# Kernel optimization log

Measured on AMD Instinct MI355X. Metric: run time of the kernel, lower is better.

Reference implementation:

```python
import jax, jax.numpy as jnp
import numpy as np

B, S, D, H = 8, 1024, 256, 16
HD = D // H  # head_dim = 16
THETA = 10000.0


def rope(x):
    # Faithful to RotaryEmbeddings: integer-division exponent, 1-indexed
    # positions, rotor = sin + i*cos (real part is sin).
    b, s, d = x.shape
    i = jnp.arange(0, d, 2)
    expo = (2 * i) // d  # integer division: 0 for first half, 1 for second
    thetas = 1.0 / (THETA ** expo.astype(jnp.float32))  # [d/2]
    pos = jnp.arange(s, dtype=jnp.float32) + 1.0  # 1-indexed positions
    ang = pos[:, None] * thetas[None, :]  # [s, d/2]
    sin, cos = jnp.sin(ang), jnp.cos(ang)
    xp = x.reshape(b, s, d // 2, 2)
    xe, xo = xp[..., 0], xp[..., 1]  # consecutive pairs (view_as_complex)
    # (xe + i*xo) * (sin + i*cos)
    real = xe * sin - xo * cos
    imag = xe * cos + xo * sin
    return jnp.stack((real, imag), axis=-1).reshape(b, s, d)


def setup_inputs() -> dict:
    key = jax.random.key(0)
    ks = jax.random.split(key, 9)
    sc = 1.0 / np.sqrt(D)
    return {
        "x": jax.random.normal(ks[0], (B, S, D), dtype=jnp.float32),
        "wq_w": jax.random.normal(ks[1], (D, D), dtype=jnp.float32) * sc,
        "wq_b": jax.random.normal(ks[2], (D,), dtype=jnp.float32) * 0.01,
        "wk_w": jax.random.normal(ks[3], (D, D), dtype=jnp.float32) * sc,
        "wk_b": jax.random.normal(ks[4], (D,), dtype=jnp.float32) * 0.01,
        "wv_w": jax.random.normal(ks[5], (D, D), dtype=jnp.float32) * sc,
        "wv_b": jax.random.normal(ks[6], (D,), dtype=jnp.float32) * 0.01,
        "wo_w": jax.random.normal(ks[7], (D, D), dtype=jnp.float32) * sc,
        "wo_b": jax.random.normal(ks[8], (D,), dtype=jnp.float32) * 0.01,
    }


def reference(x, wq_w, wq_b, wk_w, wk_b, wv_w, wv_b, wo_w, wo_b):
    b, s, d = x.shape
    q = x @ wq_w.T + wq_b
    k = x @ wk_w.T + wk_b  # computed in original but dead in no-cache path
    v = x @ wv_w.T + wv_b
    del k
    xq = rope(q).reshape(b, s, H, HD).transpose(0, 2, 1, 3)  # [b,h,s,hd]
    xv = rope(v).reshape(b, s, H, HD).transpose(0, 2, 1, 3)  # [b,h,s,hd]
    # no-cache path: keys = xq (rotated queries), values = rotated v; NO softmax
    scores = jnp.einsum('bhqd,bhkd->bhqk', xq, xq) / jnp.sqrt(jnp.float32(HD))
    att = jnp.einsum('bhqk,bhkd->bhqd', scores, xv)  # [b,h,s,hd]
    att = att.transpose(0, 2, 1, 3).reshape(b, s, d)
    return att @ wo_w.T + wo_b
```

## Files before the change

### kernel.cpp

```cpp
#include <hip/hip_runtime.h>

#define Gz 8192
#define Dz 256
#define Sz 1024

typedef _Float16 half8 __attribute__((ext_vector_type(8)));
typedef float    floatx4 __attribute__((ext_vector_type(4)));

#define GLOAD_LDS(gptr, lptr)                                                      \
    __builtin_amdgcn_global_load_lds(                                              \
        (const __attribute__((address_space(1))) void*)(gptr),                     \
        (__attribute__((address_space(3))) void*)(lptr), 16, 0, 0)

__device__ inline half8 cvt8(const float* __restrict__ p) {
    float4 a = ((const float4*)p)[0];
    float4 b = ((const float4*)p)[1];
    half8 h;
    h[0]=(_Float16)a.x; h[1]=(_Float16)a.y; h[2]=(_Float16)a.z; h[3]=(_Float16)a.w;
    h[4]=(_Float16)b.x; h[5]=(_Float16)b.y; h[6]=(_Float16)b.z; h[7]=(_Float16)b.w;
    return h;
}

__global__ __launch_bounds__(256) void convert_kernel(
    const float* __restrict__ x, const float* __restrict__ wq,
    const float* __restrict__ wv,
    _Float16* __restrict__ x16, _Float16* __restrict__ w16)
{
    size_t e = ((size_t)blockIdx.x * 256 + threadIdx.x) * 8;
    const float* src;
    _Float16* dst;
    if (e < (size_t)Gz * Dz) { src = x + e; dst = x16 + e; }
    else {
        size_t e2 = e - (size_t)Gz * Dz;
        dst = w16 + e2;
        src = (e2 < 65536) ? (wq + e2) : (wv + (e2 - 65536));
    }
    *(half8*)dst = cvt8(src);
}

__global__ __launch_bounds__(256) void qv_gemm_rope(
    const _Float16* __restrict__ x16, const _Float16* __restrict__ w16,
    const float* __restrict__ bq, const float* __restrict__ bv,
    _Float16* __restrict__ xq, _Float16* __restrict__ xv)
{
    __shared__ _Float16 As[128 * 64];
    __shared__ _Float16 Bs[128 * 64];
    const int t = threadIdx.x, lane = t & 63, w = t >> 6;
    const int g0 = blockIdx.x * 128;
    const int by = blockIdx.y;
    const int n0 = by * 128;
    const int wm = (w >> 1) * 64, wn = (w & 1) * 64;
    const int fr = lane & 15, kq = lane >> 4;

    floatx4 acc[4][4] = {};

    for (int k0 = 0; k0 < Dz; k0 += 64) {
        __syncthreads();
        #pragma unroll
        for (int p = 0; p < 4; ++p) {
            const int flat = (t + 256 * p) * 8;
            const int row = flat >> 6, col = flat & 63;
            GLOAD_LDS(x16 + (size_t)(g0 + row) * Dz + k0 + col, &As[flat]);
            GLOAD_LDS(w16 + (size_t)(n0 + row) * Dz + k0 + col, &Bs[flat]);
        }
        __syncthreads();
        #pragma unroll
        for (int ks = 0; ks < 2; ++ks) {
            const int kk = ks * 32 + kq * 8;
            half8 a[4], b[4];
            #pragma unroll
            for (int i = 0; i < 4; ++i) a[i] = *(const half8*)&As[(wm + i * 16 + fr) * 64 + kk];
            #pragma unroll
            for (int j = 0; j < 4; ++j) b[j] = *(const half8*)&Bs[(wn + j * 16 + fr) * 64 + kk];
            #pragma unroll
            for (int i = 0; i < 4; ++i)
                #pragma unroll
                for (int j = 0; j < 4; ++j)
                    acc[i][j] = __builtin_amdgcn_mfma_f32_16x16x32_f16(a[i], b[j], acc[i][j], 0, 0, 0);
        }
    }

    const int qside = (by < 2);
    const float* bias = qside ? bq : bv;
    _Float16* outp = qside ? xq : xv;
    const float theta = (by & 1) ? 1e-4f : 1.0f;
    const float sign  = (fr & 1) ? 1.0f : -1.0f;

    float sn[4][4], cs[4][4];
    #pragma unroll
    for (int i = 0; i < 4; ++i)
        #pragma unroll
        for (int r = 0; r < 4; ++r) {
            const int g = g0 + wm + i * 16 + kq * 4 + r;
            const float pos = (float)((g & (Sz - 1)) + 1);
            __sincosf(pos * theta, &sn[i][r], &cs[i][r]);
        }

    #pragma unroll
    for (int j = 0; j < 4; ++j) {
        const int ch = (by & 1) * 128 + wn + j * 16 + fr;
        const float bcol = bias[ch];
        #pragma unroll
        for (int i = 0; i < 4; ++i)
            #pragma unroll
            for (int r = 0; r < 4; ++r) {
                const int g = g0 + wm + i * 16 + kq * 4 + r;
                float v = acc[i][j][r] + bcol;
                float other = __shfl_xor(v, 1, 64);
                outp[(size_t)g * Dz + ch] =
                    (_Float16)(v * sn[i][r] + sign * other * cs[i][r]);
            }
    }
}

__global__ __launch_bounds__(256) void head_outer(
    const _Float16* __restrict__ xq, const _Float16* __restrict__ xv,
    float* __restrict__ Mpart)
{
    __shared__ __align__(16) _Float16 qsT[16][136];
    __shared__ __align__(16) _Float16 vsT[16][136];
    const int t = threadIdx.x;
    const int bh = blockIdx.x;
    const int b = bh >> 4, h = bh & 15;
    const size_t base = (size_t)b * Sz * Dz + (size_t)blockIdx.y * 128 * Dz + h * 16;

    {
        const int s = t >> 1, eg = t & 1;
        half8 q8 = *(const half8*)&xq[base + (size_t)s * Dz + eg * 8];
        half8 v8 = *(const half8*)&xv[base + (size_t)s * Dz + eg * 8];
        #pragma unroll
        for (int i = 0; i < 8; ++i) {
            qsT[eg * 8 + i][s] = q8[i];
            vsT[eg * 8 + i][s] = v8[i];
        }
    }
    __syncthreads();

    const int e = t >> 4, f = t & 15;
    float acc = 0.f;
    #pragma unroll
    for (int s0 = 0; s0 < 128; s0 += 8) {
        half8 q8 = *(const half8*)&qsT[e][s0];
        half8 v8 = *(const half8*)&vsT[f][s0];
        #pragma unroll
        for (int i = 0; i < 8; ++i) acc += (float)q8[i] * (float)v8[i];
    }
    Mpart[((size_t)blockIdx.y * 128 + bh) * 256 + t] = acc;
}

__global__ __launch_bounds__(256) void make_p(
    const float* __restrict__ Mpart, const float* __restrict__ Wo,
    _Float16* __restrict__ Pt)
{
    __shared__ float Ms[256];
    const int t = threadIdx.x;
    const int bh = blockIdx.x;
    const int b = bh >> 4, h = bh & 15;
    float s = 0.f;
    #pragma unroll
    for (int c = 0; c < 8; ++c) s += Mpart[((size_t)c * 128 + bh) * 256 + t];
    Ms[t] = s * 0.25f;
    __syncthreads();

    const int c = t;
    float wo[16];
    const float4* wop = (const float4*)&Wo[(size_t)c * Dz + h * 16];
    #pragma unroll
    for (int q = 0; q < 4; ++q) {
        float4 v = wop[q];
        wo[4*q+0] = v.x; wo[4*q+1] = v.y; wo[4*q+2] = v.z; wo[4*q+3] = v.w;
    }
    half8 lo, hi;
    #pragma unroll
    for (int e = 0; e < 16; ++e) {
        float a = 0.f;
        #pragma unroll
        for (int f = 0; f < 16; ++f) a = fmaf(Ms[e * 16 + f], wo[f], a);
        if (e < 8) lo[e] = (_Float16)a; else hi[e - 8] = (_Float16)a;
    }
    _Float16* dst = &Pt[((size_t)(b * 256 + c)) * Dz + h * 16];
    *(half8*)dst       = lo;
    *(half8*)(dst + 8) = hi;
}

__global__ __launch_bounds__(256) void out_gemm(
    const _Float16* __restrict__ xq, const _Float16* __restrict__ Pt,
    const float* __restrict__ bo, float* __restrict__ out)
{
    __shared__ _Float16 As[64 * 64];
    __shared__ _Float16 Bs[128 * 64];
    const int t = threadIdx.x, lane = t & 63, w = t >> 6;
    const int g0 = blockIdx.x * 64;
    const int n0 = blockIdx.y * 128;
    const int b  = g0 >> 10;
    const int wm = (w >> 1) * 32, wn = (w & 1) * 64;
    const int fr = lane & 15, kq = lane >> 4;
    const _Float16* Pb = Pt + (size_t)b * 256 * Dz;

    floatx4 acc[2][4] = {};

    for (int k0 = 0; k0 < Dz; k0 += 64) {
        __syncthreads();
        #pragma unroll
        for (int p = 0; p < 2; ++p) {
            const int flat = (t + 256 * p) * 8;
            const int row = flat >> 6, col = flat & 63;
            GLOAD_LDS(xq + (size_t)(g0 + row) * Dz + k0 + col, &As[flat]);
        }
        #pragma unroll
        for (int p = 0; p < 4; ++p) {
            const int flat = (t + 256 * p) * 8;
            const int row = flat >> 6, col = flat & 63;
            GLOAD_LDS(Pb + (size_t)(n0 + row) * Dz + k0 + col, &Bs[flat]);
        }
        __syncthreads();
        #pragma unroll
        for (int ks = 0; ks < 2; ++ks) {
            const int kk = ks * 32 + kq * 8;
            half8 a[2], bf[4];
            #pragma unroll
            for (int i = 0; i < 2; ++i) a[i] = *(const half8*)&As[(wm + i * 16 + fr) * 64 + kk];
            #pragma unroll
            for (int j = 0; j < 4; ++j) bf[j] = *(const half8*)&Bs[(wn + j * 16 + fr) * 64 + kk];
            #pragma unroll
            for (int i = 0; i < 2; ++i)
                #pragma unroll
                for (int j = 0; j < 4; ++j)
                    acc[i][j] = __builtin_amdgcn_mfma_f32_16x16x32_f16(a[i], bf[j], acc[i][j], 0, 0, 0);
        }
    }

    #pragma unroll
    for (int j = 0; j < 4; ++j) {
        const int c = n0 + wn + j * 16 + fr;
        const float bcol = bo[c];
        #pragma unroll
        for (int i = 0; i < 2; ++i)
            #pragma unroll
            for (int r = 0; r < 4; ++r) {
                const int g = g0 + wm + i * 16 + kq * 4 + r;
                out[(size_t)g * Dz + c] = acc[i][j][r] + bcol;
            }
    }
}

extern "C" void kernel_launch(void* const* d_in, const int* in_sizes, int n_in,
                              void* d_out, int out_size, void* d_ws, size_t ws_size,
                              hipStream_t stream)
{
    const float* x    = (const float*)d_in[0];
    const float* wq_w = (const float*)d_in[1];
    const float* wq_b = (const float*)d_in[2];
    const float* wv_w = (const float*)d_in[5];
    const float* wv_b = (const float*)d_in[6];
    const float* wo_w = (const float*)d_in[7];
    const float* wo_b = (const float*)d_in[8];

    _Float16* x16  = (_Float16*)d_ws;
    _Float16* w16  = x16  + (size_t)Gz * Dz;
    _Float16* xq16 = w16  + 131072;
    _Float16* xv16 = xq16 + (size_t)Gz * Dz;
    _Float16* Pt   = xv16 + (size_t)Gz * Dz;
    float*    Mpart = (float*)(Pt + 524288);
    float*    out  = (float*)d_out;

    convert_kernel<<<dim3((Gz * Dz + 131072) / 2048), 256, 0, stream>>>(
        x, wq_w, wv_w, x16, w16);
    qv_gemm_rope<<<dim3(Gz / 128, 4), 256, 0, stream>>>(
        x16, w16, wq_b, wv_b, xq16, xv16);
    head_outer<<<dim3(128, 8), 256, 0, stream>>>(xq16, xv16, Mpart);
    make_p<<<dim3(128), 256, 0, stream>>>(Mpart, wo_w, Pt);
    out_gemm<<<dim3(Gz / 64, 2), 256, 0, stream>>>(xq16, Pt, wo_b, out);
}
```

Baseline: 102.7 us.

## Fuse per-head outer product and Wo projection into one kernel

Merges the head_outer and make_p kernels into a single kernel. Each block loops over all eight sequence chunks and accumulates the 16x16 per-head matrix in registers, then multiplies it by Wo directly. This removes one kernel launch and the Mpart global round trip. The cost is far less parallelism: 128 blocks instead of 1024, with the chunk loads serialized inside each block.

Measured after the change: 105.8 us. 3.0% more time.

```diff
diff --git a/kernel.cpp b/kernel.cpp
--- a/kernel.cpp
+++ b/kernel.cpp
@@ -113,53 +113,46 @@
     }
 }
 
-__global__ __launch_bounds__(256) void head_outer(
+__global__ __launch_bounds__(256) void headm_p(
     const _Float16* __restrict__ xq, const _Float16* __restrict__ xv,
-    float* __restrict__ Mpart)
+    const float* __restrict__ Wo, _Float16* __restrict__ Pt)
 {
     __shared__ __align__(16) _Float16 qsT[16][136];
     __shared__ __align__(16) _Float16 vsT[16][136];
-    const int t = threadIdx.x;
-    const int bh = blockIdx.x;
-    const int b = bh >> 4, h = bh & 15;
-    const size_t base = (size_t)b * Sz * Dz + (size_t)blockIdx.y * 128 * Dz + h * 16;
-
-    {
-        const int s = t >> 1, eg = t & 1;
-        half8 q8 = *(const half8*)&xq[base + (size_t)s * Dz + eg * 8];
-        half8 v8 = *(const half8*)&xv[base + (size_t)s * Dz + eg * 8];
-        #pragma unroll
-        for (int i = 0; i < 8; ++i) {
-            qsT[eg * 8 + i][s] = q8[i];
-            vsT[eg * 8 + i][s] = v8[i];
-        }
-    }
-    __syncthreads();
-
-    const int e = t >> 4, f = t & 15;
-    float acc = 0.f;
-    #pragma unroll
-    for (int s0 = 0; s0 < 128; s0 += 8) {
-        half8 q8 = *(const half8*)&qsT[e][s0];
-        half8 v8 = *(const half8*)&vsT[f][s0];
-        #pragma unroll
-        for (int i = 0; i < 8; ++i) acc += (float)q8[i] * (float)v8[i];
-    }
-    Mpart[((size_t)blockIdx.y * 128 + bh) * 256 + t] = acc;
-}
-
-__global__ __launch_bounds__(256) void make_p(
-    const float* __restrict__ Mpart, const float* __restrict__ Wo,
-    _Float16* __restrict__ Pt)
-{
     __shared__ float Ms[256];
     const int t = threadIdx.x;
     const int bh = blockIdx.x;
     const int b = bh >> 4, h = bh & 15;
-    float s = 0.f;
-    #pragma unroll
-    for (int c = 0; c < 8; ++c) s += Mpart[((size_t)c * 128 + bh) * 256 + t];
-    Ms[t] = s * 0.25f;
+    const size_t base0 = (size_t)b * Sz * Dz + h * 16;
+
+    const int e = t >> 4, f = t & 15;
+    float acc = 0.f;
+
+    for (int chunk = 0; chunk < 8; ++chunk) {
+        const size_t base = base0 + (size_t)chunk * 128 * Dz;
+        __syncthreads();
+        {
+            const int s = t >> 1, eg = t & 1;
+            half8 q8 = *(const half8*)&xq[base + (size_t)s * Dz + eg * 8];
+            half8 v8 = *(const half8*)&xv[base + (size_t)s * Dz + eg * 8];
+            #pragma unroll
+            for (int i = 0; i < 8; ++i) {
+                qsT[eg * 8 + i][s] = q8[i];
+                vsT[eg * 8 + i][s] = v8[i];
+            }
+        }
+        __syncthreads();
+        #pragma unroll
+        for (int s0 = 0; s0 < 128; s0 += 8) {
+            half8 q8 = *(const half8*)&qsT[e][s0];
+            half8 v8 = *(const half8*)&vsT[f][s0];
+            #pragma unroll
+            for (int i = 0; i < 8; ++i) acc += (float)q8[i] * (float)v8[i];
+        }
+    }
+
+    __syncthreads();
+    Ms[t] = acc * 0.25f;
     __syncthreads();
 
     const int c = t;
@@ -172,11 +165,11 @@
     }
     half8 lo, hi;
     #pragma unroll
-    for (int e = 0; e < 16; ++e) {
+    for (int ee = 0; ee < 16; ++ee) {
         float a = 0.f;
         #pragma unroll
-        for (int f = 0; f < 16; ++f) a = fmaf(Ms[e * 16 + f], wo[f], a);
-        if (e < 8) lo[e] = (_Float16)a; else hi[e - 8] = (_Float16)a;
+        for (int ff = 0; ff < 16; ++ff) a = fmaf(Ms[ee * 16 + ff], wo[ff], a);
+        if (ee < 8) lo[ee] = (_Float16)a; else hi[ee - 8] = (_Float16)a;
     }
     _Float16* dst = &Pt[((size_t)(b * 256 + c)) * Dz + h * 16];
     *(half8*)dst       = lo;
@@ -261,14 +254,12 @@
     _Float16* xq16 = w16  + 131072;
     _Float16* xv16 = xq16 + (size_t)Gz * Dz;
     _Float16* Pt   = xv16 + (size_t)Gz * Dz;
-    float*    Mpart = (float*)(Pt + 524288);
     float*    out  = (float*)d_out;
 
     convert_kernel<<<dim3((Gz * Dz + 131072) / 2048), 256, 0, stream>>>(
         x, wq_w, wv_w, x16, w16);
     qv_gemm_rope<<<dim3(Gz / 128, 4), 256, 0, stream>>>(
         x16, w16, wq_b, wv_b, xq16, xv16);
-    head_outer<<<dim3(128, 8), 256, 0, stream>>>(xq16, xv16, Mpart);
-    make_p<<<dim3(128), 256, 0, stream>>>(Mpart, wo_w, Pt);
+    headm_p<<<dim3(128), 256, 0, stream>>>(xq16, xv16, wo_w, Pt);
     out_gemm<<<dim3(Gz / 64, 2), 256, 0, stream>>>(xq16, Pt, wo_b, out);
 }
```
